# Kernel tuning notes

Hardware: AMD Instinct MI355X
Metric: run time of the kernel (lower is better)

The kernel has to match this reference:

```python
import jax, jax.numpy as jnp
import numpy as np

B, N, DIM, H, DH = 8, 1024, 512, 8, 64
INNER = H * DH
SCALE = DH ** -0.5
EPS = 1e-12  # F.normalize eps


def setup_inputs() -> dict:
    key = jax.random.key(0)
    k1, k2, k3, k4, k5 = jax.random.split(key, 5)
    x = jax.random.normal(k1, (B, N, DIM), dtype=jnp.float32)
    spd = jax.random.normal(k2, (B, 1, N, N), dtype=jnp.float32)
    # per-head binomial keep mask (one realized draw of the original loop), guaranteed nonzero
    a = np.random.RandomState(0).binomial(1, 0.9, size=H)
    if a.sum() == 0:
        a[0] = 1
    head_mask = jnp.asarray(a, dtype=jnp.float32)
    W_qkv = jax.random.normal(k3, (DIM, 3 * INNER), dtype=jnp.float32) * (DIM ** -0.5)
    W_out = jax.random.normal(k4, (INNER, DIM), dtype=jnp.float32) * (INNER ** -0.5)
    b_out = jax.random.normal(k5, (DIM,), dtype=jnp.float32) * 0.01
    return {"x": x, "spd": spd, "head_mask": head_mask,
            "W_qkv": W_qkv, "W_out": W_out, "b_out": b_out}


def reference(x, spd, head_mask, W_qkv, W_out, b_out):
    b, n, _ = x.shape
    qkv = x @ W_qkv                                   # [b, n, 3*inner]
    q, k, v = jnp.split(qkv, 3, axis=-1)
    split_heads = lambda t: t.reshape(b, n, H, DH).transpose(0, 2, 1, 3)  # b h n d
    q, k, v = split_heads(q), split_heads(k), split_heads(v)

    dots = jnp.einsum('bhnd,bhmd->bhnm', q, k) * SCALE        # [b,h,n,n]
    prod = dots * spd                                         # broadcast spd over heads
    prod_norm = jnp.sqrt(jnp.sum(prod * prod, axis=-1, keepdims=True))
    dots_norm = jnp.sqrt(jnp.sum(dots * dots, axis=-1, keepdims=True))
    bias = prod / jnp.maximum(prod_norm, EPS) * dots_norm     # F.normalize(prod)*||dots||
    attn = jax.nn.softmax(dots + bias, axis=-1)

    # head dropout mask with rescale: attn * mask * H / sum(mask)
    scale_m = head_mask * (H / jnp.sum(head_mask))
    attn = attn * scale_m[None, :, None, None]

    out = jnp.einsum('bhnm,bhmd->bhnd', attn, v)              # [b,h,n,d]
    out = out.transpose(0, 2, 1, 3).reshape(b, n, INNER)      # b n (h d)
    return out @ W_out + b_out
```

## Files before the change

kernel.cpp:

```cpp
#include <hip/hip_runtime.h>
#include <hip/hip_bf16.h>

typedef __attribute__((ext_vector_type(8))) short short8;
typedef __attribute__((ext_vector_type(4))) short s16x4;
typedef __attribute__((ext_vector_type(4))) float f32x4;

typedef const __attribute__((address_space(1))) unsigned* gp1;
typedef __attribute__((address_space(3))) unsigned* lp3;

__device__ inline short f2bf(float f) {
    union { float f; unsigned u; } v; v.f = f;
    unsigned r = v.u + 0x7fffu + ((v.u >> 16) & 1u);
    return (short)(r >> 16);
}

__global__ __launch_bounds__(256) void cvt_bf16(
    const float* __restrict__ src, short* __restrict__ dst, int n4)
{
    int i = blockIdx.x * 256 + threadIdx.x;
    if (i < n4) {
        float4 v = ((const float4*)src)[i];
        s16x4 o = { f2bf(v.x), f2bf(v.y), f2bf(v.z), f2bf(v.w) };
        ((s16x4*)dst)[i] = o;
    }
}

__global__ __launch_bounds__(256) void tr_w(
    const float* __restrict__ src, short* __restrict__ dst, int K, int N)
{
    __shared__ float t[64][65];
    const int k0 = blockIdx.x * 64, n0 = blockIdx.y * 64;
    const int r = threadIdx.x >> 4, c4 = (threadIdx.x & 15) * 4;
#pragma unroll
    for (int j = 0; j < 4; j++) {
        float4 v = *(const float4*)(src + (size_t)(k0 + r + 16 * j) * N + n0 + c4);
        t[r + 16 * j][c4 + 0] = v.x; t[r + 16 * j][c4 + 1] = v.y;
        t[r + 16 * j][c4 + 2] = v.z; t[r + 16 * j][c4 + 3] = v.w;
    }
    __syncthreads();
#pragma unroll
    for (int j = 0; j < 4; j++) {
        const int n = r + 16 * j;
        s16x4 o = { f2bf(t[c4 + 0][n]), f2bf(t[c4 + 1][n]),
                    f2bf(t[c4 + 2][n]), f2bf(t[c4 + 3][n]) };
        *(s16x4*)(dst + (size_t)(n0 + n) * K + k0 + c4) = o;
    }
}

__global__ __launch_bounds__(256) void qkv_gemm(
    const short* __restrict__ A, const short* __restrict__ BT,
    short* __restrict__ q, short* __restrict__ k, short* __restrict__ vt)
{
    __shared__ short sA[128][32];
    __shared__ short sB[128][32];

    const int tid  = threadIdx.x;
    const int wv   = tid >> 6, lane = tid & 63;
    const int quad = lane >> 4, l16 = lane & 15;
    const int wr = wv >> 1, wc = wv & 1;
    const int m0 = blockIdx.x * 128, n0 = blockIdx.y * 128;

    f32x4 acc[4][4];
#pragma unroll
    for (int i = 0; i < 4; i++)
#pragma unroll
        for (int j = 0; j < 4; j++) acc[i][j] = (f32x4){0.f, 0.f, 0.f, 0.f};

    const short* a_src = A  + (size_t)(m0 + wv * 32 + (lane >> 2)) * 512 + (lane & 3) * 8;
    const short* b_src = BT + (size_t)(n0 + wv * 32 + (lane >> 2)) * 512 + (lane & 3) * 8;
    char* a_dst = (char*)sA + wv * 2048;
    char* b_dst = (char*)sB + wv * 2048;

    for (int ks = 0; ks < 16; ks++) {
        __syncthreads();
        const short* ap = a_src + ks * 32;
        const short* bp = b_src + ks * 32;
        __builtin_amdgcn_global_load_lds((gp1)(ap),            (lp3)(a_dst),        16, 0, 0);
        __builtin_amdgcn_global_load_lds((gp1)(ap + 16 * 512), (lp3)(a_dst + 1024), 16, 0, 0);
        __builtin_amdgcn_global_load_lds((gp1)(bp),            (lp3)(b_dst),        16, 0, 0);
        __builtin_amdgcn_global_load_lds((gp1)(bp + 16 * 512), (lp3)(b_dst + 1024), 16, 0, 0);
        __syncthreads();

        short8 af[4], bf[4];
#pragma unroll
        for (int f = 0; f < 4; f++) {
            af[f] = *(const short8*)&sA[wr * 64 + f * 16 + l16][quad * 8];
            bf[f] = *(const short8*)&sB[wc * 64 + f * 16 + l16][quad * 8];
        }
#pragma unroll
        for (int fm = 0; fm < 4; fm++)
#pragma unroll
            for (int fn = 0; fn < 4; fn++)
                acc[fm][fn] = __builtin_amdgcn_mfma_f32_16x16x32_bf16(
                    af[fm], bf[fn], acc[fm][fn], 0, 0, 0);
    }

    const int sec = n0 >> 9;
#pragma unroll
    for (int fn = 0; fn < 4; fn++) {
        const int gc = n0 + wc * 64 + fn * 16 + l16;
        const int cc = gc & 511;
        const int h = cc >> 6, d = cc & 63;
#pragma unroll
        for (int fm = 0; fm < 4; fm++)
#pragma unroll
            for (int i = 0; i < 4; i++) {
                const int gm = m0 + wr * 64 + fm * 16 + quad * 4 + i;
                const int b = gm >> 10, n = gm & 1023;
                const int bh = b * 8 + h;
                if (sec == 0)      q[((size_t)(bh * 1024 + n)) * 64 + d] = f2bf(acc[fm][fn][i] * 0.125f);
                else if (sec == 1) k[((size_t)(bh * 1024 + n)) * 64 + d] = f2bf(acc[fm][fn][i]);
                else               vt[((size_t)(bh * 64 + d)) * 1024 + n] = f2bf(acc[fm][fn][i]);
            }
    }
}

__global__ __launch_bounds__(256, 4) void attn_k(
    const short* __restrict__ q, const short* __restrict__ kk,
    const short* __restrict__ vt, const float* __restrict__ spd,
    const float* __restrict__ hm, short* __restrict__ o)
{
    __shared__ short sK[64][72];
    __shared__ short sV[64][72];
    __shared__ short sP[4][16][72];
    __shared__ float sred[4][16];

    const int tid  = threadIdx.x;
    const int wv   = tid >> 6, lane = tid & 63;
    const int quad = lane >> 4, l16 = lane & 15;
    const int qt = blockIdx.x, bh = blockIdx.y;
    const int b = bh >> 3, h = bh & 7;
    const int q0 = qt * 64;

    const short* qb = q + ((size_t)bh * 1024 + q0 + wv * 16 + l16) * 64;
    short8 aq0 = *(const short8*)(qb + quad * 8);
    short8 aq1 = *(const short8*)(qb + 32 + quad * 8);

    const int sr = tid & 31, sc = (tid >> 5) * 8;
    const short* ksrc = kk + (size_t)bh * 65536 + (size_t)sr * 64 + sc;
    const short* vsrc = vt + (size_t)bh * 65536 + (size_t)sr * 1024 + sc;
    const float* sp   = spd + ((size_t)b * 1024 + q0 + wv * 16 + l16) * 1024 + quad * 4;

    float dn = 0.f, pn = 0.f;
    short8 k0 = *(const short8*)(ksrc);
    short8 k1 = *(const short8*)(ksrc + 2048);
    float4 sv0 = *(const float4*)(sp +  0);
    float4 sv1 = *(const float4*)(sp + 16);
    float4 sv2 = *(const float4*)(sp + 32);
    float4 sv3 = *(const float4*)(sp + 48);

    for (int c = 0; c < 16; ++c) {
        __syncthreads();
        *(short8*)&sK[sr][sc]      = k0;
        *(short8*)&sK[sr + 32][sc] = k1;
        __syncthreads();
        float4 svc0 = sv0, svc1 = sv1, svc2 = sv2, svc3 = sv3;
        if (c < 15) {
            k0 = *(const short8*)(ksrc + (c + 1) * 4096);
            k1 = *(const short8*)(ksrc + (c + 1) * 4096 + 2048);
            sv0 = *(const float4*)(sp + (c + 1) * 64 +  0);
            sv1 = *(const float4*)(sp + (c + 1) * 64 + 16);
            sv2 = *(const float4*)(sp + (c + 1) * 64 + 32);
            sv3 = *(const float4*)(sp + (c + 1) * 64 + 48);
        }
        f32x4 a[4];
#pragma unroll
        for (int t = 0; t < 4; t++) {
            a[t] = (f32x4){0.f, 0.f, 0.f, 0.f};
            a[t] = __builtin_amdgcn_mfma_f32_16x16x32_bf16(
                *(const short8*)&sK[t * 16 + l16][quad * 8], aq0, a[t], 0, 0, 0);
            a[t] = __builtin_amdgcn_mfma_f32_16x16x32_bf16(
                *(const short8*)&sK[t * 16 + l16][32 + quad * 8], aq1, a[t], 0, 0, 0);
        }
        const float4 svv[4] = {svc0, svc1, svc2, svc3};
#pragma unroll
        for (int t = 0; t < 4; t++)
#pragma unroll
            for (int i = 0; i < 4; i++) {
                float s  = a[t][i];
                float sv = ((const float*)&svv[t])[i];
                float ps = s * sv;
                dn = fmaf(s, s, dn);
                pn = fmaf(ps, ps, pn);
            }
    }
    dn += __shfl_xor(dn, 16, 64); dn += __shfl_xor(dn, 32, 64);
    pn += __shfl_xor(pn, 16, 64); pn += __shfl_xor(pn, 32, 64);
    const float ratio = sqrtf(dn) / fmaxf(sqrtf(pn), 1e-12f);

    float m_r = -1e30f, ls = 0.f;
    f32x4 O[4];
#pragma unroll
    for (int dt = 0; dt < 4; dt++) O[dt] = (f32x4){0.f, 0.f, 0.f, 0.f};

    k0 = *(const short8*)(ksrc);
    k1 = *(const short8*)(ksrc + 2048);
    short8 v0 = *(const short8*)(vsrc);
    short8 v1 = *(const short8*)(vsrc + 32768);

    for (int c = 0; c < 16; ++c) {
        __syncthreads();
        *(short8*)&sK[sr][sc]      = k0;
        *(short8*)&sK[sr + 32][sc] = k1;
        *(short8*)&sV[sr][sc]      = v0;
        *(short8*)&sV[sr + 32][sc] = v1;
        __syncthreads();
        float4 svc0 = *(const float4*)(sp + c * 64 +  0);
        float4 svc1 = *(const float4*)(sp + c * 64 + 16);
        float4 svc2 = *(const float4*)(sp + c * 64 + 32);
        float4 svc3 = *(const float4*)(sp + c * 64 + 48);
        if (c < 15) {
            k0 = *(const short8*)(ksrc + (c + 1) * 4096);
            k1 = *(const short8*)(ksrc + (c + 1) * 4096 + 2048);
            v0 = *(const short8*)(vsrc + (c + 1) * 64);
            v1 = *(const short8*)(vsrc + (c + 1) * 64 + 32768);
        }
        f32x4 a[4];
#pragma unroll
        for (int t = 0; t < 4; t++) {
            a[t] = (f32x4){0.f, 0.f, 0.f, 0.f};
            a[t] = __builtin_amdgcn_mfma_f32_16x16x32_bf16(
                *(const short8*)&sK[t * 16 + l16][quad * 8], aq0, a[t], 0, 0, 0);
            a[t] = __builtin_amdgcn_mfma_f32_16x16x32_bf16(
                *(const short8*)&sK[t * 16 + l16][32 + quad * 8], aq1, a[t], 0, 0, 0);
        }
        const float4 svv[4] = {svc0, svc1, svc2, svc3};
        float mx = -1e30f;
#pragma unroll
        for (int t = 0; t < 4; t++)
#pragma unroll
            for (int i = 0; i < 4; i++) {
                float s  = a[t][i];
                float sv = ((const float*)&svv[t])[i];
                float l  = s * fmaf(sv, ratio, 1.0f);
                a[t][i] = l;
                mx = fmaxf(mx, l);
            }
        mx = fmaxf(mx, __shfl_xor(mx, 16, 64));
        mx = fmaxf(mx, __shfl_xor(mx, 32, 64));
        const float m_new = fmaxf(m_r, mx);
        const float fo = __expf(m_r - m_new);
        m_r = m_new;
        ls *= fo;
        float fov[4];
#pragma unroll
        for (int i = 0; i < 4; i++) fov[i] = __shfl(fo, quad * 4 + i, 16);
#pragma unroll
        for (int dt = 0; dt < 4; dt++) {
            O[dt][0] *= fov[0]; O[dt][1] *= fov[1];
            O[dt][2] *= fov[2]; O[dt][3] *= fov[3];
        }
#pragma unroll
        for (int t = 0; t < 4; t++) {
            float p0 = __expf(a[t][0] - m_r);
            float p1 = __expf(a[t][1] - m_r);
            float p2 = __expf(a[t][2] - m_r);
            float p3 = __expf(a[t][3] - m_r);
            ls += (p0 + p1) + (p2 + p3);
            s16x4 pk = { f2bf(p0), f2bf(p1), f2bf(p2), f2bf(p3) };
            *(s16x4*)&sP[wv][l16][t * 16 + quad * 4] = pk;
        }
#pragma unroll
        for (int kc = 0; kc < 2; kc++) {
            short8 pa = *(const short8*)&sP[wv][l16][kc * 32 + quad * 8];
#pragma unroll
            for (int dt = 0; dt < 4; dt++) {
                short8 vf = *(const short8*)&sV[dt * 16 + l16][kc * 32 + quad * 8];
                O[dt] = __builtin_amdgcn_mfma_f32_16x16x32_bf16(pa, vf, O[dt], 0, 0, 0);
            }
        }
    }
    ls += __shfl_xor(ls, 16, 64); ls += __shfl_xor(ls, 32, 64);
    const float hsum = hm[0] + hm[1] + hm[2] + hm[3] + hm[4] + hm[5] + hm[6] + hm[7];
    const float rinv = hm[h] * 8.0f / (hsum * ls);
    if (quad == 0) sred[wv][l16] = rinv;
    __syncthreads();
    float rv[4];
#pragma unroll
    for (int i = 0; i < 4; i++) rv[i] = sred[wv][quad * 4 + i];
#pragma unroll
    for (int dt = 0; dt < 4; dt++)
#pragma unroll
        for (int i = 0; i < 4; i++)
            o[((size_t)(b * 1024 + q0 + wv * 16 + quad * 4 + i)) * 512 + h * 64 + dt * 16 + l16]
                = f2bf(O[dt][i] * rv[i]);
}

__global__ __launch_bounds__(256) void out_gemm(
    const short* __restrict__ A, const short* __restrict__ BT,
    const float* __restrict__ bias, float* __restrict__ out)
{
    __shared__ short sA[128][32];
    __shared__ short sB[128][32];

    const int tid  = threadIdx.x;
    const int wv   = tid >> 6, lane = tid & 63;
    const int quad = lane >> 4, l16 = lane & 15;
    const int wr = wv >> 1, wc = wv & 1;
    const int m0 = blockIdx.x * 128, n0 = blockIdx.y * 128;

    f32x4 acc[4][4];
#pragma unroll
    for (int i = 0; i < 4; i++)
#pragma unroll
        for (int j = 0; j < 4; j++) acc[i][j] = (f32x4){0.f, 0.f, 0.f, 0.f};

    const short* a_src = A  + (size_t)(m0 + wv * 32 + (lane >> 2)) * 512 + (lane & 3) * 8;
    const short* b_src = BT + (size_t)(n0 + wv * 32 + (lane >> 2)) * 512 + (lane & 3) * 8;
    char* a_dst = (char*)sA + wv * 2048;
    char* b_dst = (char*)sB + wv * 2048;

    for (int ks = 0; ks < 16; ks++) {
        __syncthreads();
        const short* ap = a_src + ks * 32;
        const short* bp = b_src + ks * 32;
        __builtin_amdgcn_global_load_lds((gp1)(ap),            (lp3)(a_dst),        16, 0, 0);
        __builtin_amdgcn_global_load_lds((gp1)(ap + 16 * 512), (lp3)(a_dst + 1024), 16, 0, 0);
        __builtin_amdgcn_global_load_lds((gp1)(bp),            (lp3)(b_dst),        16, 0, 0);
        __builtin_amdgcn_global_load_lds((gp1)(bp + 16 * 512), (lp3)(b_dst + 1024), 16, 0, 0);
        __syncthreads();

        short8 af[4], bf[4];
#pragma unroll
        for (int f = 0; f < 4; f++) {
            af[f] = *(const short8*)&sA[wr * 64 + f * 16 + l16][quad * 8];
            bf[f] = *(const short8*)&sB[wc * 64 + f * 16 + l16][quad * 8];
        }
#pragma unroll
        for (int fm = 0; fm < 4; fm++)
#pragma unroll
            for (int fn = 0; fn < 4; fn++)
                acc[fm][fn] = __builtin_amdgcn_mfma_f32_16x16x32_bf16(
                    af[fm], bf[fn], acc[fm][fn], 0, 0, 0);
    }

#pragma unroll
    for (int fn = 0; fn < 4; fn++) {
        const int gc = n0 + wc * 64 + fn * 16 + l16;
        const float bv = bias[gc];
#pragma unroll
        for (int fm = 0; fm < 4; fm++)
#pragma unroll
            for (int i = 0; i < 4; i++) {
                const int gm = m0 + wr * 64 + fm * 16 + quad * 4 + i;
                out[(size_t)gm * 512 + gc] = acc[fm][fn][i] + bv;
            }
    }
}

extern "C" void kernel_launch(void* const* d_in, const int* in_sizes, int n_in,
                              void* d_out, int out_size, void* d_ws, size_t ws_size,
                              hipStream_t stream) {
    const float* x    = (const float*)d_in[0];
    const float* spd  = (const float*)d_in[1];
    const float* hm   = (const float*)d_in[2];
    const float* Wqkv = (const float*)d_in[3];
    const float* Wout = (const float*)d_in[4];
    const float* bout = (const float*)d_in[5];
    float* out = (float*)d_out;

    char* ws = (char*)d_ws;
    short* qw  = (short*)(ws);
    short* kw  = (short*)(ws + ((size_t)8  << 20));
    short* vtw = (short*)(ws + ((size_t)16 << 20));
    short* ow  = (short*)(ws + ((size_t)24 << 20));
    short* xb  = (short*)(ws + ((size_t)32 << 20));
    short* wqT = (short*)(ws + ((size_t)40 << 20));
    short* woT = (short*)(ws + ((size_t)42 << 20));

    cvt_bf16<<<4096, 256, 0, stream>>>(x, xb, 8192 * 512 / 4);
    tr_w    <<<dim3(8, 24), 256, 0, stream>>>(Wqkv, wqT, 512, 1536);
    tr_w    <<<dim3(8, 8),  256, 0, stream>>>(Wout, woT, 512, 512);

    qkv_gemm<<<dim3(64, 12), 256, 0, stream>>>(xb, wqT, qw, kw, vtw);
    attn_k  <<<dim3(16, 64), 256, 0, stream>>>(qw, kw, vtw, spd, hm, ow);
    out_gemm<<<dim3(64, 4),  256, 0, stream>>>(ow, woT, bout, out);
}
```

Before: 250.2 us.

## Replace online softmax with precomputed per-row max bound from norm pass

The first pass that computes row norms now also tracks the per-row max of the scores and of the score*spd products. From these it forms an upper bound Mhat on the logit, used as a fixed softmax offset. This drops the per-chunk max reduction, cross-lane shuffles, rescale exponent and O accumulator rescaling from the second pass. The bound is loose (max(s) + ratio*max(s*sv)), so the exponents can underflow when it greatly exceeds the true max, which is a precision risk.

```diff
diff --git a/kernel.cpp b/kernel.cpp
--- a/kernel.cpp
+++ b/kernel.cpp
@@ -141,7 +141,7 @@
     const short* vsrc = vt + (size_t)bh * 65536 + (size_t)sr * 1024 + sc;
     const float* sp   = spd + ((size_t)b * 1024 + q0 + wv * 16 + l16) * 1024 + quad * 4;
 
-    float dn = 0.f, pn = 0.f;
+    float dn = 0.f, pn = 0.f, mxs = -1e30f, mxp = -1e30f;
     short8 k0 = *(const short8*)(ksrc);
     short8 k1 = *(const short8*)(ksrc + 2048);
     float4 sv0 = *(const float4*)(sp +  0);
@@ -182,13 +182,18 @@
                 float ps = s * sv;
                 dn = fmaf(s, s, dn);
                 pn = fmaf(ps, ps, pn);
-            }
-    }
-    dn += __shfl_xor(dn, 16, 64); dn += __shfl_xor(dn, 32, 64);
-    pn += __shfl_xor(pn, 16, 64); pn += __shfl_xor(pn, 32, 64);
+                mxs = fmaxf(mxs, s);
+                mxp = fmaxf(mxp, ps);
+            }
+    }
+    dn  += __shfl_xor(dn, 16, 64);  dn  += __shfl_xor(dn, 32, 64);
+    pn  += __shfl_xor(pn, 16, 64);  pn  += __shfl_xor(pn, 32, 64);
+    mxs = fmaxf(mxs, __shfl_xor(mxs, 16, 64)); mxs = fmaxf(mxs, __shfl_xor(mxs, 32, 64));
+    mxp = fmaxf(mxp, __shfl_xor(mxp, 16, 64)); mxp = fmaxf(mxp, __shfl_xor(mxp, 32, 64));
     const float ratio = sqrtf(dn) / fmaxf(sqrtf(pn), 1e-12f);
-
-    float m_r = -1e30f, ls = 0.f;
+    const float Mhat  = mxs + ratio * mxp;
+
+    float ls = 0.f;
     f32x4 O[4];
 #pragma unroll
     for (int dt = 0; dt < 4; dt++) O[dt] = (f32x4){0.f, 0.f, 0.f, 0.f};
@@ -225,37 +230,25 @@
                 *(const short8*)&sK[t * 16 + l16][32 + quad * 8], aq1, a[t], 0, 0, 0);
         }
         const float4 svv[4] = {svc0, svc1, svc2, svc3};
-        float mx = -1e30f;
-#pragma unroll
-        for (int t = 0; t < 4; t++)
-#pragma unroll
-            for (int i = 0; i < 4; i++) {
-                float s  = a[t][i];
-                float sv = ((const float*)&svv[t])[i];
-                float l  = s * fmaf(sv, ratio, 1.0f);
-                a[t][i] = l;
-                mx = fmaxf(mx, l);
-            }
-        mx = fmaxf(mx, __shfl_xor(mx, 16, 64));
-        mx = fmaxf(mx, __shfl_xor(mx, 32, 64));
-        const float m_new = fmaxf(m_r, mx);
-        const float fo = __expf(m_r - m_new);
-        m_r = m_new;
-        ls *= fo;
-        float fov[4];
-#pragma unroll
-        for (int i = 0; i < 4; i++) fov[i] = __shfl(fo, quad * 4 + i, 16);
-#pragma unroll
-        for (int dt = 0; dt < 4; dt++) {
-            O[dt][0] *= fov[0]; O[dt][1] *= fov[1];
-            O[dt][2] *= fov[2]; O[dt][3] *= fov[3];
-        }
 #pragma unroll
         for (int t = 0; t < 4; t++) {
-            float p0 = __expf(a[t][0] - m_r);
-            float p1 = __expf(a[t][1] - m_r);
-            float p2 = __expf(a[t][2] - m_r);
-            float p3 = __expf(a[t][3] - m_r);
+            float p0, p1, p2, p3;
+            {
+                float s = a[t][0], sv = ((const float*)&svv[t])[0];
+                p0 = __expf(s * fmaf(sv, ratio, 1.0f) - Mhat);
+            }
+            {
+                float s = a[t][1], sv = ((const float*)&svv[t])[1];
+                p1 = __expf(s * fmaf(sv, ratio, 1.0f) - Mhat);
+            }
+            {
+                float s = a[t][2], sv = ((const float*)&svv[t])[2];
+                p2 = __expf(s * fmaf(sv, ratio, 1.0f) - Mhat);
+            }
+            {
+                float s = a[t][3], sv = ((const float*)&svv[t])[3];
+                p3 = __expf(s * fmaf(sv, ratio, 1.0f) - Mhat);
+            }
             ls += (p0 + p1) + (p2 + p3);
             s16x4 pk = { f2bf(p0), f2bf(p1), f2bf(p2), f2bf(p3) };
             *(s16x4*)&sP[wv][l16][t * 16 + quad * 4] = pk;
```

Result: no change. 247.8 us (-1.0%).
